# Performance work log

Measured on AMD Instinct MI355X. Metric: run time of the kernel, lower is better.

Reference implementation:

```python
import jax, jax.numpy as jnp
import numpy as np
from itertools import combinations

N_QUBITS = 8
PAIRS = list(combinations(range(N_QUBITS), 2))  # 28 qubit pairs -> 28 features/node

# qubit 0 = first tensor factor (most significant bit of the basis index)
CNOT01 = jnp.array([[1,0,0,0],[0,1,0,0],[0,0,0,1],[0,0,1,0]], dtype=jnp.complex64)  # control q0, target q1
CNOT10 = jnp.array([[1,0,0,0],[0,0,0,1],[0,0,1,0],[0,1,0,0]], dtype=jnp.complex64)  # control q1, target q0
I2 = jnp.eye(2, dtype=jnp.complex64)
HZ = jnp.array([1.0, -1.0, 1.0, -1.0], dtype=jnp.complex64)  # diag(I kron Z)


def _rx(t):
    c = jnp.cos(t / 2).astype(jnp.complex64)
    s = jnp.sin(t / 2).astype(jnp.complex64)
    return jnp.stack([jnp.stack([c, -1j * s]), jnp.stack([-1j * s, c])])


def _ry(t):
    c = jnp.cos(t / 2).astype(jnp.complex64)
    s = jnp.sin(t / 2).astype(jnp.complex64)
    return jnp.stack([jnp.stack([c, -s]), jnp.stack([s, c])])


def _rz(t):
    e = jnp.exp(-0.5j * t.astype(jnp.complex64))
    z = jnp.zeros((), jnp.complex64)
    return jnp.stack([jnp.stack([e, z]), jnp.stack([z, jnp.conj(e)])])


def _pair_unitary(p):  # p: [6] params for one qubit pair
    A = _rz(p[5]) @ _ry(p[4]) @ _rx(p[3]) @ _rz(p[2]) @ _ry(p[1]) @ _rx(p[0])
    return CNOT01 @ (CNOT10 @ jnp.kron(A, I2))  # [4,4]


def _quantum_features(x, qweight):
    """Batched version of the per-node amplitude encoding + 28 two-qubit circuits."""
    N = x.shape[0]
    psi = (x / jnp.linalg.norm(x, axis=1, keepdims=True)).astype(jnp.complex64)  # [N,256]
    psi8 = psi.reshape((N,) + (2,) * N_QUBITS)
    Us = jax.vmap(_pair_unitary)(qweight.reshape(len(PAIRS), 6))  # [28,4,4]
    cols = []
    for p, (a, b) in enumerate(PAIRS):
        perm = (0, 1 + a, 1 + b) + tuple(1 + q for q in range(N_QUBITS) if q not in (a, b))
        v = jnp.transpose(psi8, perm).reshape(N, 4, 2 ** (N_QUBITS - 2))  # [N,4,64]
        rho = jnp.einsum('nim,njm->nij', v, jnp.conj(v))  # reduced 2-qubit DM [N,4,4]
        U = Us[p]
        # <I kron Z> after U rho U^dagger, mapped to [0,1]
        e = jnp.einsum('a,ab,nbc,ac->n', HZ, U, rho, jnp.conj(U))
        cols.append((jnp.real(e) + 1.0) * 0.5)
    return jnp.stack(cols, axis=1).astype(jnp.float32)  # [N,28]


def reference(x, edge_index, qweight, W1, b1, W2, b2):
    N = x.shape[0]
    x_deal = _quantum_features(x, qweight)  # [N,28]
    # gcn_norm with added self loops, edge_weight = 1
    loop = jnp.arange(N)
    src = jnp.concatenate([edge_index[0], loop])
    dst = jnp.concatenate([edge_index[1], loop])
    w = jnp.ones(src.shape[0], dtype=jnp.float32)
    deg = jax.ops.segment_sum(w, dst, num_segments=N)
    dinv = jax.lax.rsqrt(jnp.maximum(deg, 1e-12))
    norm = dinv[src] * w * dinv[dst]
    out = jax.ops.segment_sum(norm[:, None] * x_deal[src], dst, num_segments=N)  # [N,28]
    out = jax.nn.relu(out)
    g = (out.T @ out).reshape(1, 28 * 28)  # [1,784]
    h = jax.nn.relu(g @ W1.T + b1)
    return jax.nn.sigmoid(h @ W2.T + b2)  # [1,1]


def setup_inputs() -> dict:
    N, F, E = 50000, 256, 1600000
    key = jax.random.key(0)
    ks = jax.random.split(key, 6)
    x = jax.random.normal(ks[0], (N, F), dtype=jnp.float32)
    edge_index = jax.random.randint(ks[1], (2, E), 0, N, dtype=jnp.int64)
    qweight = jax.random.uniform(ks[2], (168,), dtype=jnp.float32) * (2.0 * np.pi)
    W1 = jax.random.normal(ks[3], (128, 784), dtype=jnp.float32) * 0.03
    b1 = jnp.zeros((128,), dtype=jnp.float32)
    W2 = jax.random.normal(ks[4], (1, 128), dtype=jnp.float32) * 0.08
    b2 = jnp.zeros((1,), dtype=jnp.float32)
    return {"x": x, "edge_index": edge_index, "qweight": qweight,
            "W1": W1, "b1": b1, "W2": W2, "b2": b2}
```

## Files before the change

kernel.cpp:

```cpp
#include <hip/hip_runtime.h>
#include <hip/hip_fp16.h>
#include <math.h>

#define N_NODES 50000
#define N_EDGES 1600000
#define BSHIFT 6
#define NB_BUCKETS 782
#define PART_CHUNK 8192
#define NCHUNK 196
#define CAP 3072
#define ZSTRIDE 32

template<int CTRL>
__device__ inline float dpp_mov(float x){
    return __int_as_float(__builtin_amdgcn_update_dpp(0, __float_as_int(x), CTRL, 0xf, 0xf, false));
}
__device__ inline float wave_sum_dpp(float x){
    x += dpp_mov<0x111>(x);
    x += dpp_mov<0x112>(x);
    x += dpp_mov<0x114>(x);
    x += dpp_mov<0x118>(x);
    x += dpp_mov<0x142>(x);
    x += dpp_mov<0x143>(x);
    return x;
}
__device__ inline float lane63(float x){
    return __int_as_float(__builtin_amdgcn_readlane(__float_as_int(x), 63));
}
#define DPP_XOR1 0xB1
#define DPP_XOR2 0x4E

struct C2 { float x, y; };
__device__ inline C2 mkc(float x, float y){ C2 r; r.x=x; r.y=y; return r; }
__device__ inline C2 cmul(C2 a, C2 b){ return mkc(a.x*b.x - a.y*b.y, a.x*b.y + a.y*b.x); }
__device__ inline C2 cadd(C2 a, C2 b){ return mkc(a.x+b.x, a.y+b.y); }

__global__ __launch_bounds__(256) void k_init(const float* __restrict__ qw,
        const void* __restrict__ ei, float4* __restrict__ cmat,
        int* __restrict__ flag, int* __restrict__ bucketFill, float* __restrict__ G){
    int t = threadIdx.x;
    for (int i = t; i < NB_BUCKETS; i += 256) bucketFill[i] = 0;
    for (int i = t; i < 784; i += 256) G[i] = 0.f;
    if (t == 255){
        const long long* e64 = (const long long*)ei;
        int ok = 1;
        for (int i = 0; i < 64; i++){
            long long v = e64[i];
            if (v < 0 || v >= N_NODES) ok = 0;
        }
        flag[0] = ok;
    }
    if (t < 28){
        int p = t;
        int a = 0; { int rem = p, q = 0; while (rem >= 7 - q){ rem -= 7 - q; q++; } a = q; }
        C2 M00 = mkc(1,0), M01 = mkc(0,0), M10 = mkc(0,0), M11 = mkc(1,0);
        for (int k = 0; k < 6; k++){
            float th = 0.5f * qw[p*6 + k];
            float s, c; sincosf(th, &s, &c);
            C2 R00, R01, R10, R11;
            int type = k % 3;
            if (type == 0){
                R00 = mkc(c,0); R01 = mkc(0,-s); R10 = mkc(0,-s); R11 = mkc(c,0);
            } else if (type == 1){
                R00 = mkc(c,0); R01 = mkc(-s,0); R10 = mkc(s,0); R11 = mkc(c,0);
            } else {
                R00 = mkc(c,-s); R01 = mkc(0,0); R10 = mkc(0,0); R11 = mkc(c,s);
            }
            C2 N00 = cadd(cmul(R00,M00), cmul(R01,M10));
            C2 N01 = cadd(cmul(R00,M01), cmul(R01,M11));
            C2 N10 = cadd(cmul(R10,M00), cmul(R11,M10));
            C2 N11 = cadd(cmul(R10,M01), cmul(R11,M11));
            M00=N00; M01=N01; M10=N10; M11=N11;
        }
        float B00  = (M00.x*M00.x + M00.y*M00.y) - (M10.x*M10.x + M10.y*M10.y);
        float B11  = (M01.x*M01.x + M01.y*M01.y) - (M11.x*M11.x + M11.y*M11.y);
        float B01r = (M00.x*M01.x + M00.y*M01.y) - (M10.x*M11.x + M10.y*M11.y);
        cmat[p] = make_float4(0.5f + 0.5f*B11, 0.5f*(B00 - B11), B01r, (float)a);
    }
}

__device__ inline int get_edge(const void* ei, int is64, long long idx){
    if (is64) return (int)((const long long*)ei)[idx];
    return ((const int*)ei)[idx];
}

__global__ __launch_bounds__(1024) void k_part(const void* __restrict__ ei,
        const int* __restrict__ flag, int* __restrict__ bucketFill,
        unsigned* __restrict__ pairs){
    __shared__ int hist[NB_BUCKETS];
    __shared__ int cntb[NB_BUCKETS];
    __shared__ int cursor[NB_BUCKETS];
    __shared__ int copyBase[NB_BUCKETS];
    __shared__ unsigned sorted[PART_CHUNK];
    int tid = threadIdx.x, c = blockIdx.x;
    long long base = (long long)c * PART_CHUNK;
    int cnt = (int)((N_EDGES - base < PART_CHUNK) ? (N_EDGES - base) : PART_CHUNK);
    int is64 = flag[0];
    unsigned ds[8], sr[8];
    #pragma unroll
    for (int k = 0; k < 8; k++){
        int i = tid + 1024*k;
        if (i < cnt){
            ds[k] = (unsigned)get_edge(ei, is64, (long long)N_EDGES + base + i);
            sr[k] = (unsigned)get_edge(ei, is64, base + i);
        } else ds[k] = 0xffffffffu;
    }
    if (tid < NB_BUCKETS) hist[tid] = 0;
    __syncthreads();
    #pragma unroll
    for (int k = 0; k < 8; k++)
        if (ds[k] != 0xffffffffu) atomicAdd(&hist[ds[k] >> BSHIFT], 1);
    __syncthreads();
    if (tid < NB_BUCKETS) cntb[tid] = hist[tid];
    __syncthreads();
    for (int ofs = 1; ofs < NB_BUCKETS; ofs <<= 1){
        int v = 0; bool a = tid < NB_BUCKETS;
        if (a) v = hist[tid] + (tid >= ofs ? hist[tid - ofs] : 0);
        __syncthreads();
        if (a) hist[tid] = v;
        __syncthreads();
    }
    if (tid < NB_BUCKETS){
        int cb = cntb[tid];
        int ls = hist[tid] - cb;
        int gbase = tid*CAP + atomicAdd(&bucketFill[tid], cb);
        copyBase[tid] = gbase - ls;
        cursor[tid] = ls;
    }
    __syncthreads();
    #pragma unroll
    for (int k = 0; k < 8; k++){
        if (ds[k] != 0xffffffffu){
            int pos = atomicAdd(&cursor[ds[k] >> BSHIFT], 1);
            sorted[pos] = (ds[k] << 16) | sr[k];
        }
    }
    __syncthreads();
    for (int i = tid; i < cnt; i += 1024){
        unsigned v = sorted[i];
        int b = (int)(v >> 22);
        pairs[copyBase[b] + i] = v;
    }
}

__global__ __launch_bounds__(256) void k_sort(const unsigned* __restrict__ pairs,
        const int* __restrict__ bucketFill, unsigned short* __restrict__ csr,
        int* __restrict__ nodeOff, float* __restrict__ dinv){
    __shared__ unsigned short sorted[CAP];
    __shared__ int hist[64];
    __shared__ int cursor[64];
    int b = blockIdx.x, t = threadIdx.x;
    int s0 = b*CAP;
    int cnt = bucketFill[b];
    if (cnt > CAP) cnt = CAP;
    if (t < 64) hist[t] = 0;
    __syncthreads();
    for (int i = t; i < cnt; i += 256){
        unsigned v = pairs[s0 + i];
        atomicAdd(&hist[(v >> 16) & 63], 1);
    }
    __syncthreads();
    int mycnt = (t < 64) ? hist[t] : 0;
    for (int ofs = 1; ofs < 64; ofs <<= 1){
        int nv = 0;
        if (t < 64) nv = hist[t] + (t >= ofs ? hist[t - ofs] : 0);
        __syncthreads();
        if (t < 64) hist[t] = nv;
        __syncthreads();
    }
    if (t < 64){
        cursor[t] = hist[t] - mycnt;
        int n = b*64 + t;
        if (n < N_NODES){
            nodeOff[n] = s0 + hist[t] - mycnt;
            dinv[n] = rsqrtf((float)(mycnt + 1));
        }
    }
    __syncthreads();
    for (int i = t; i < cnt; i += 256){
        unsigned v = pairs[s0 + i];
        int d = (v >> 16) & 63;
        int pos = atomicAdd(&cursor[d], 1);
        sorted[pos] = (unsigned short)(v & 0xffffu);
    }
    __syncthreads();
    for (int i = t; i < cnt; i += 256) csr[s0 + i] = sorted[i];
}

__global__ __launch_bounds__(256) void k_feat(const float* __restrict__ x,
        const float* __restrict__ dinv, const float4* __restrict__ cmat,
        __half* __restrict__ z){
    int wave = threadIdx.x >> 6;
    int lane = threadIdx.x & 63;
    int n = blockIdx.x*4 + wave;
    const float4 v = ((const float4*)(x + (size_t)n*256))[lane];
    float persq = v.x*v.x + v.y*v.y + v.z*v.z + v.w*v.w;

    float red[15];
    red[0] = persq;
    red[1] = v.x*v.x + v.y*v.y;
    red[2] = v.x*v.z + v.y*v.w;
    {
        float px = dpp_mov<DPP_XOR1>(v.x), py = dpp_mov<DPP_XOR1>(v.y);
        float pz = dpp_mov<DPP_XOR1>(v.z), pw = dpp_mov<DPP_XOR1>(v.w);
        red[3] = v.x*px + v.y*py + v.z*pz + v.w*pw;
        red[9] = (lane & 1) ? 0.f : persq;
    }
    {
        float px = dpp_mov<DPP_XOR2>(v.x), py = dpp_mov<DPP_XOR2>(v.y);
        float pz = dpp_mov<DPP_XOR2>(v.z), pw = dpp_mov<DPP_XOR2>(v.w);
        red[4] = v.x*px + v.y*py + v.z*pz + v.w*pw;
        red[10] = (lane & 2) ? 0.f : persq;
    }
    #pragma unroll
    for (int j = 2; j < 6; j++){
        float px = __shfl_xor(v.x, 1 << j), py = __shfl_xor(v.y, 1 << j);
        float pz = __shfl_xor(v.z, 1 << j), pw = __shfl_xor(v.w, 1 << j);
        red[3 + j] = v.x*px + v.y*py + v.z*pz + v.w*pw;
        red[9 + j] = ((lane >> j) & 1) ? 0.0f : persq;
    }
    float S[15];
    #pragma unroll
    for (int k = 0; k < 15; k++) S[k] = lane63(wave_sum_dpp(red[k]));

    if (lane < 28){
        float4 cm = cmat[lane];
        int ap = (int)cm.w;
        float S0a = (ap==6) ? S[1] :
                    (ap==0 ? S[14] : ap==1 ? S[13] : ap==2 ? S[12] :
                     ap==3 ? S[11] : ap==4 ? S[10] : S[9]);
        float Xa  = (ap==6) ? S[2] :
                    0.5f*(ap==0 ? S[8] : ap==1 ? S[7] : ap==2 ? S[6] :
                          ap==3 ? S[5] : ap==4 ? S[4] : S[3]);
        float feat = cm.x + (cm.y*S0a + cm.z*Xa) / S[0];
        z[(size_t)n*ZSTRIDE + lane] = __float2half(dinv[n] * feat);
    } else if (lane < 32){
        z[(size_t)n*ZSTRIDE + lane] = __float2half(0.f);
    }
}

__device__ inline void acc_pack(unsigned u, float& a, float& b){
    float2 f = __half22float2(__builtin_bit_cast(__half2, u));
    a += f.x; b += f.y;
}
__device__ inline void acc_row(const uint4* rp, float* acc ){
    uint4 w0 = rp[0], w1 = rp[1], w2 = rp[2], w3 = rp[3];
    acc_pack(w0.x, acc[0],  acc[1]);  acc_pack(w0.y, acc[2],  acc[3]);
    acc_pack(w0.z, acc[4],  acc[5]);  acc_pack(w0.w, acc[6],  acc[7]);
    acc_pack(w1.x, acc[8],  acc[9]);  acc_pack(w1.y, acc[10], acc[11]);
    acc_pack(w1.z, acc[12], acc[13]); acc_pack(w1.w, acc[14], acc[15]);
    acc_pack(w2.x, acc[16], acc[17]); acc_pack(w2.y, acc[18], acc[19]);
    acc_pack(w2.z, acc[20], acc[21]); acc_pack(w2.w, acc[22], acc[23]);
    acc_pack(w3.x, acc[24], acc[25]); acc_pack(w3.y, acc[26], acc[27]);
    acc_pack(w3.z, acc[28], acc[29]); acc_pack(w3.w, acc[30], acc[31]);
}

__global__ __launch_bounds__(256) void k_gather(const unsigned short* __restrict__ csr,
        const int* __restrict__ nodeOff, const int* __restrict__ bucketFill,
        const __half* __restrict__ z, const float* __restrict__ dinv,
        float* __restrict__ out){
    int g = blockIdx.x*256 + threadIdx.x;
    int n = g >> 2, sub = g & 3;
    if (n >= N_NODES) return;
    int b = n >> 6, d = n & 63;
    int beg = nodeOff[n];
    int end = (d == 63 || n == N_NODES - 1) ? b*CAP + min(bucketFill[b], CAP)
                                            : nodeOff[n + 1];
    float acc[32];
    #pragma unroll
    for (int k = 0; k < 32; k++) acc[k] = 0.f;
    for (int i = beg + sub; i < end; i += 4){
        int src = csr[i];
        acc_row((const uint4*)(z + (size_t)src*ZSTRIDE), acc);
    }
    if (sub == 3) acc_row((const uint4*)(z + (size_t)n*ZSTRIDE), acc);
    #pragma unroll
    for (int k = 0; k < 32; k++){
        acc[k] += dpp_mov<DPP_XOR1>(acc[k]);
        acc[k] += dpp_mov<DPP_XOR2>(acc[k]);
    }
    if (sub == 0){
        float dv = dinv[n];
        float4* o = (float4*)(out + (size_t)n*28);
        #pragma unroll
        for (int q = 0; q < 7; q++)
            o[q] = make_float4(fmaxf(acc[4*q+0]*dv, 0.f), fmaxf(acc[4*q+1]*dv, 0.f),
                               fmaxf(acc[4*q+2]*dv, 0.f), fmaxf(acc[4*q+3]*dv, 0.f));
    }
}

__global__ __launch_bounds__(256) void k_gram(const float* __restrict__ out, float* __restrict__ G){
    __shared__ float buf[64*28];
    int tid = threadIdx.x;
    bool val = tid < 196;
    int ti = val ? tid / 14 : 0, tj = val ? tid % 14 : 0;
    int i0 = 2*ti, j0 = 2*tj;
    float c00 = 0.f, c01 = 0.f, c10 = 0.f, c11 = 0.f;
    int nchunks = (N_NODES + 63) / 64;
    for (int ch = blockIdx.x; ch < nchunks; ch += gridDim.x){
        int base = ch * 64;
        int total = (N_NODES - base < 64 ? N_NODES - base : 64) * 28;
        __syncthreads();
        for (int t = tid; t < 64*28; t += 256)
            buf[t] = (t < total) ? out[(size_t)base*28 + t] : 0.f;
        __syncthreads();
        for (int nn = 0; nn < 64; nn++){
            const float* r = buf + nn*28;
            float a0 = r[i0], a1 = r[i0+1], b0 = r[j0], b1 = r[j0+1];
            c00 += a0*b0; c01 += a0*b1; c10 += a1*b0; c11 += a1*b1;
        }
    }
    if (val){
        atomicAdd(&G[(i0  )*28 + j0  ], c00);
        atomicAdd(&G[(i0  )*28 + j0+1], c01);
        atomicAdd(&G[(i0+1)*28 + j0  ], c10);
        atomicAdd(&G[(i0+1)*28 + j0+1], c11);
    }
}

__global__ __launch_bounds__(256) void k_mlp(const float* __restrict__ G,
        const float* __restrict__ W1, const float* __restrict__ b1,
        const float* __restrict__ W2, const float* __restrict__ b2,
        float* __restrict__ outp){
    __shared__ float part[256];
    __shared__ float h[128];
    int t = threadIdx.x;
    int j = t & 127, halfsel = t >> 7;
    const float* w = W1 + (size_t)j*784 + halfsel*392;
    const float* g = G + halfsel*392;
    float s = 0.f;
    for (int i = 0; i < 392; i++) s += g[i] * w[i];
    part[t] = s;
    __syncthreads();
    if (t < 128) h[t] = fmaxf(part[t] + part[t+128] + b1[t], 0.f) * W2[t];
    __syncthreads();
    for (int ofs = 64; ofs > 0; ofs >>= 1){
        if (t < ofs) h[t] += h[t + ofs];
        __syncthreads();
    }
    if (t == 0) outp[0] = 1.f / (1.f + expf(-(h[0] + b2[0])));
}

extern "C" void kernel_launch(void* const* d_in, const int* in_sizes, int n_in,
                              void* d_out, int out_size, void* d_ws, size_t ws_size,
                              hipStream_t stream){
    const float* x  = (const float*)d_in[0];
    const void*  ei = d_in[1];
    const float* qw = (const float*)d_in[2];
    const float* W1 = (const float*)d_in[3];
    const float* b1 = (const float*)d_in[4];
    const float* W2 = (const float*)d_in[5];
    const float* b2 = (const float*)d_in[6];
    float* outp = (float*)d_out;

    char* base = (char*)d_ws;
    __half*         z     = (__half*)base;         base += (size_t)N_NODES*ZSTRIDE*2;
    float*          ob    = (float*)base;          base += (size_t)N_NODES*28*4;
    unsigned*       pairs = (unsigned*)base;       base += (size_t)NB_BUCKETS*CAP*4;
    unsigned short* csr   = (unsigned short*)base; base += (size_t)NB_BUCKETS*CAP*2;
    int*            nodeOff = (int*)base;          base += (size_t)N_NODES*4;
    float*          dinv  = (float*)base;          base += (size_t)N_NODES*4;
    float4*         cmat  = (float4*)base;         base += 448;
    float*          G     = (float*)base;          base += 4096;
    int*            bucketFill = (int*)base;       base += 4096;
    int*            flag  = (int*)base;            base += 16;

    k_init<<<1, 256, 0, stream>>>(qw, ei, cmat, flag, bucketFill, G);
    k_part<<<NCHUNK, 1024, 0, stream>>>(ei, flag, bucketFill, pairs);
    k_sort<<<NB_BUCKETS, 256, 0, stream>>>(pairs, bucketFill, csr, nodeOff, dinv);
    k_feat<<<N_NODES/4, 256, 0, stream>>>(x, dinv, cmat, z);
    k_gather<<<(N_NODES*4 + 255)/256, 256, 0, stream>>>(csr, nodeOff, bucketFill, z, dinv, ob);
    k_gram<<<196, 256, 0, stream>>>(ob, G);
    k_mlp<<<1, 256, 0, stream>>>(G, W1, b1, W2, b2, outp);
}
```

Baseline: 209.7 us.

## Fuse gather, gram and MLP into one kernel; halve partition chunk

Fuses neighbor aggregation, per-block Gram accumulation and the final MLP into a single kernel. Each block computes relu-normalized rows into shared memory, accumulates its 64-node Gram tile with global atomics, and the last block to finish (via a done counter) runs the MLP. This removes the intermediate output buffer round trip and two kernel launches, at the cost of many more atomics into G. Separately, the partition kernel uses 4096-edge chunks with 512 threads for more blocks.

New measurement: 273.8 us. 1.31x slower.

```diff
diff --git a/kernel.cpp b/kernel.cpp
--- a/kernel.cpp
+++ b/kernel.cpp
@@ -6,8 +6,8 @@
 #define N_EDGES 1600000
 #define BSHIFT 6
 #define NB_BUCKETS 782
-#define PART_CHUNK 8192
-#define NCHUNK 196
+#define PART_CHUNK 4096
+#define NCHUNK 391
 #define CAP 3072
 #define ZSTRIDE 32
 
@@ -37,10 +37,12 @@
 
 __global__ __launch_bounds__(256) void k_init(const float* __restrict__ qw,
         const void* __restrict__ ei, float4* __restrict__ cmat,
-        int* __restrict__ flag, int* __restrict__ bucketFill, float* __restrict__ G){
+        int* __restrict__ flag, int* __restrict__ bucketFill, float* __restrict__ G,
+        int* __restrict__ done){
     int t = threadIdx.x;
     for (int i = t; i < NB_BUCKETS; i += 256) bucketFill[i] = 0;
     for (int i = t; i < 784; i += 256) G[i] = 0.f;
+    if (t == 254) done[0] = 0;
     if (t == 255){
         const long long* e64 = (const long long*)ei;
         int ok = 1;
@@ -84,7 +86,7 @@
     return ((const int*)ei)[idx];
 }
 
-__global__ __launch_bounds__(1024) void k_part(const void* __restrict__ ei,
+__global__ __launch_bounds__(512) void k_part(const void* __restrict__ ei,
         const int* __restrict__ flag, int* __restrict__ bucketFill,
         unsigned* __restrict__ pairs){
     __shared__ int hist[NB_BUCKETS];
@@ -99,33 +101,37 @@
     unsigned ds[8], sr[8];
     #pragma unroll
     for (int k = 0; k < 8; k++){
-        int i = tid + 1024*k;
+        int i = tid + 512*k;
         if (i < cnt){
             ds[k] = (unsigned)get_edge(ei, is64, (long long)N_EDGES + base + i);
             sr[k] = (unsigned)get_edge(ei, is64, base + i);
         } else ds[k] = 0xffffffffu;
     }
-    if (tid < NB_BUCKETS) hist[tid] = 0;
+    for (int i = tid; i < NB_BUCKETS; i += 512) hist[i] = 0;
     __syncthreads();
     #pragma unroll
     for (int k = 0; k < 8; k++)
         if (ds[k] != 0xffffffffu) atomicAdd(&hist[ds[k] >> BSHIFT], 1);
     __syncthreads();
-    if (tid < NB_BUCKETS) cntb[tid] = hist[tid];
+    for (int i = tid; i < NB_BUCKETS; i += 512) cntb[i] = hist[i];
     __syncthreads();
     for (int ofs = 1; ofs < NB_BUCKETS; ofs <<= 1){
-        int v = 0; bool a = tid < NB_BUCKETS;
-        if (a) v = hist[tid] + (tid >= ofs ? hist[tid - ofs] : 0);
-        __syncthreads();
-        if (a) hist[tid] = v;
-        __syncthreads();
-    }
-    if (tid < NB_BUCKETS){
-        int cb = cntb[tid];
-        int ls = hist[tid] - cb;
-        int gbase = tid*CAP + atomicAdd(&bucketFill[tid], cb);
-        copyBase[tid] = gbase - ls;
-        cursor[tid] = ls;
+        int i0 = tid, i1 = tid + 512;
+        bool a0 = i0 < NB_BUCKETS, a1 = i1 < NB_BUCKETS;
+        int v0 = 0, v1 = 0;
+        if (a0) v0 = hist[i0] + (i0 >= ofs ? hist[i0 - ofs] : 0);
+        if (a1) v1 = hist[i1] + (i1 >= ofs ? hist[i1 - ofs] : 0);
+        __syncthreads();
+        if (a0) hist[i0] = v0;
+        if (a1) hist[i1] = v1;
+        __syncthreads();
+    }
+    for (int i = tid; i < NB_BUCKETS; i += 512){
+        int cb = cntb[i];
+        int ls = hist[i] - cb;
+        int gbase = i*CAP + atomicAdd(&bucketFill[i], cb);
+        copyBase[i] = gbase - ls;
+        cursor[i] = ls;
     }
     __syncthreads();
     #pragma unroll
@@ -136,7 +142,7 @@
         }
     }
     __syncthreads();
-    for (int i = tid; i < cnt; i += 1024){
+    for (int i = tid; i < cnt; i += 512){
         unsigned v = sorted[i];
         int b = (int)(v >> 22);
         pairs[copyBase[b] + i] = v;
@@ -255,90 +261,83 @@
     acc_pack(w3.z, acc[28], acc[29]); acc_pack(w3.w, acc[30], acc[31]);
 }
 
-__global__ __launch_bounds__(256) void k_gather(const unsigned short* __restrict__ csr,
+__global__ __launch_bounds__(256) void k_gg(const unsigned short* __restrict__ csr,
         const int* __restrict__ nodeOff, const int* __restrict__ bucketFill,
         const __half* __restrict__ z, const float* __restrict__ dinv,
-        float* __restrict__ out){
-    int g = blockIdx.x*256 + threadIdx.x;
-    int n = g >> 2, sub = g & 3;
-    if (n >= N_NODES) return;
-    int b = n >> 6, d = n & 63;
-    int beg = nodeOff[n];
-    int end = (d == 63 || n == N_NODES - 1) ? b*CAP + min(bucketFill[b], CAP)
-                                            : nodeOff[n + 1];
+        float* __restrict__ G, const float* __restrict__ W1,
+        const float* __restrict__ b1, const float* __restrict__ W2,
+        const float* __restrict__ b2, float* __restrict__ outp,
+        int* __restrict__ done){
+    __shared__ float smem[64*29];
+    __shared__ int lastFlag;
+    int b = blockIdx.x, t = threadIdx.x;
+    int d = t >> 2, sub = t & 3;
+    int n = b*64 + d;
     float acc[32];
     #pragma unroll
     for (int k = 0; k < 32; k++) acc[k] = 0.f;
-    for (int i = beg + sub; i < end; i += 4){
-        int src = csr[i];
-        acc_row((const uint4*)(z + (size_t)src*ZSTRIDE), acc);
-    }
-    if (sub == 3) acc_row((const uint4*)(z + (size_t)n*ZSTRIDE), acc);
-    #pragma unroll
-    for (int k = 0; k < 32; k++){
+    float dv = 0.f;
+    if (n < N_NODES){
+        int beg = nodeOff[n];
+        int end = (d == 63 || n == N_NODES - 1) ? b*CAP + min(bucketFill[b], CAP)
+                                                : nodeOff[n + 1];
+        for (int i = beg + sub; i < end; i += 4){
+            int src = csr[i];
+            acc_row((const uint4*)(z + (size_t)src*ZSTRIDE), acc);
+        }
+        if (sub == 3) acc_row((const uint4*)(z + (size_t)n*ZSTRIDE), acc);
+        dv = dinv[n];
+    }
+    #pragma unroll
+    for (int k = 0; k < 28; k++){
         acc[k] += dpp_mov<DPP_XOR1>(acc[k]);
         acc[k] += dpp_mov<DPP_XOR2>(acc[k]);
     }
-    if (sub == 0){
-        float dv = dinv[n];
-        float4* o = (float4*)(out + (size_t)n*28);
-        #pragma unroll
-        for (int q = 0; q < 7; q++)
-            o[q] = make_float4(fmaxf(acc[4*q+0]*dv, 0.f), fmaxf(acc[4*q+1]*dv, 0.f),
-                               fmaxf(acc[4*q+2]*dv, 0.f), fmaxf(acc[4*q+3]*dv, 0.f));
-    }
-}
-
-__global__ __launch_bounds__(256) void k_gram(const float* __restrict__ out, float* __restrict__ G){
-    __shared__ float buf[64*28];
-    int tid = threadIdx.x;
-    bool val = tid < 196;
-    int ti = val ? tid / 14 : 0, tj = val ? tid % 14 : 0;
-    int i0 = 2*ti, j0 = 2*tj;
-    float c00 = 0.f, c01 = 0.f, c10 = 0.f, c11 = 0.f;
-    int nchunks = (N_NODES + 63) / 64;
-    for (int ch = blockIdx.x; ch < nchunks; ch += gridDim.x){
-        int base = ch * 64;
-        int total = (N_NODES - base < 64 ? N_NODES - base : 64) * 28;
-        __syncthreads();
-        for (int t = tid; t < 64*28; t += 256)
-            buf[t] = (t < total) ? out[(size_t)base*28 + t] : 0.f;
-        __syncthreads();
+    #pragma unroll
+    for (int k = sub*7; k < sub*7 + 7; k++)
+        smem[d*29 + k] = (n < N_NODES) ? fmaxf(acc[k]*dv, 0.f) : 0.f;
+    __syncthreads();
+    if (t < 196){
+        int ti = t / 14, tj = t % 14;
+        int i0 = 2*ti, j0 = 2*tj;
+        float c00 = 0.f, c01 = 0.f, c10 = 0.f, c11 = 0.f;
         for (int nn = 0; nn < 64; nn++){
-            const float* r = buf + nn*28;
+            const float* r = smem + nn*29;
             float a0 = r[i0], a1 = r[i0+1], b0 = r[j0], b1 = r[j0+1];
             c00 += a0*b0; c01 += a0*b1; c10 += a1*b0; c11 += a1*b1;
         }
-    }
-    if (val){
         atomicAdd(&G[(i0  )*28 + j0  ], c00);
         atomicAdd(&G[(i0  )*28 + j0+1], c01);
         atomicAdd(&G[(i0+1)*28 + j0  ], c10);
         atomicAdd(&G[(i0+1)*28 + j0+1], c11);
     }
-}
-
-__global__ __launch_bounds__(256) void k_mlp(const float* __restrict__ G,
-        const float* __restrict__ W1, const float* __restrict__ b1,
-        const float* __restrict__ W2, const float* __restrict__ b2,
-        float* __restrict__ outp){
-    __shared__ float part[256];
-    __shared__ float h[128];
-    int t = threadIdx.x;
-    int j = t & 127, halfsel = t >> 7;
-    const float* w = W1 + (size_t)j*784 + halfsel*392;
-    const float* g = G + halfsel*392;
+    __threadfence();
+    __syncthreads();
+    if (t == 0){
+        int tk = atomicAdd(done, 1);
+        lastFlag = (tk == (int)gridDim.x - 1);
+    }
+    __syncthreads();
+    if (!lastFlag) return;
+    float* Gsh  = smem;
+    float* part = smem + 784;
+    float* hh   = smem + 1040;
+    for (int i = t; i < 784; i += 256) Gsh[i] = atomicAdd(&G[i], 0.0f);
+    __syncthreads();
+    int j = t & 127, hs = t >> 7;
+    const float* w = W1 + (size_t)j*784 + hs*392;
+    const float* g = Gsh + hs*392;
     float s = 0.f;
     for (int i = 0; i < 392; i++) s += g[i] * w[i];
     part[t] = s;
     __syncthreads();
-    if (t < 128) h[t] = fmaxf(part[t] + part[t+128] + b1[t], 0.f) * W2[t];
+    if (t < 128) hh[t] = fmaxf(part[t] + part[t+128] + b1[t], 0.f) * W2[t];
     __syncthreads();
     for (int ofs = 64; ofs > 0; ofs >>= 1){
-        if (t < ofs) h[t] += h[t + ofs];
-        __syncthreads();
-    }
-    if (t == 0) outp[0] = 1.f / (1.f + expf(-(h[0] + b2[0])));
+        if (t < ofs) hh[t] += hh[t + ofs];
+        __syncthreads();
+    }
+    if (t == 0) outp[0] = 1.f / (1.f + expf(-(hh[0] + b2[0])));
 }
 
 extern "C" void kernel_launch(void* const* d_in, const int* in_sizes, int n_in,
@@ -355,7 +354,6 @@
 
     char* base = (char*)d_ws;
     __half*         z     = (__half*)base;         base += (size_t)N_NODES*ZSTRIDE*2;
-    float*          ob    = (float*)base;          base += (size_t)N_NODES*28*4;
     unsigned*       pairs = (unsigned*)base;       base += (size_t)NB_BUCKETS*CAP*4;
     unsigned short* csr   = (unsigned short*)base; base += (size_t)NB_BUCKETS*CAP*2;
     int*            nodeOff = (int*)base;          base += (size_t)N_NODES*4;
@@ -364,12 +362,12 @@
     float*          G     = (float*)base;          base += 4096;
     int*            bucketFill = (int*)base;       base += 4096;
     int*            flag  = (int*)base;            base += 16;
-
-    k_init<<<1, 256, 0, stream>>>(qw, ei, cmat, flag, bucketFill, G);
-    k_part<<<NCHUNK, 1024, 0, stream>>>(ei, flag, bucketFill, pairs);
+    int*            done  = (int*)base;            base += 16;
+
+    k_init<<<1, 256, 0, stream>>>(qw, ei, cmat, flag, bucketFill, G, done);
+    k_part<<<NCHUNK, 512, 0, stream>>>(ei, flag, bucketFill, pairs);
     k_sort<<<NB_BUCKETS, 256, 0, stream>>>(pairs, bucketFill, csr, nodeOff, dinv);
     k_feat<<<N_NODES/4, 256, 0, stream>>>(x, dinv, cmat, z);
-    k_gather<<<(N_NODES*4 + 255)/256, 256, 0, stream>>>(csr, nodeOff, bucketFill, z, dinv, ob);
-    k_gram<<<196, 256, 0, stream>>>(ob, G);
-    k_mlp<<<1, 256, 0, stream>>>(G, W1, b1, W2, b2, outp);
-}
+    k_gg<<<NB_BUCKETS, 256, 0, stream>>>(csr, nodeOff, bucketFill, z, dinv, G,
+                                         W1, b1, W2, b2, outp, done);
+}
```
